# Performance work log

Hardware: AMD Instinct MI355X
Metric: run time of the kernel (lower is better)

The kernel has to match this reference:

```python
import jax, jax.numpy as jnp
import numpy as np

NUM_CODES = 8192
DIM = 512
COMMITMENT_COST = 0.25


def setup_inputs() -> dict:
    key = jax.random.key(0)
    kx, kc = jax.random.split(key)
    x = jax.random.normal(kx, (8, 4096, DIM), dtype=jnp.float32)
    # nn.init.uniform_(codebook.weight, -1/num_codes, 1/num_codes)
    bound = 1.0 / NUM_CODES
    codebook = jax.random.uniform(kc, (NUM_CODES, DIM), dtype=jnp.float32,
                                  minval=-bound, maxval=bound)
    return {"x": x, "codebook": codebook}


def reference(x, codebook):
    orig_shape = x.shape
    flat = x.reshape(-1, orig_shape[-1])              # [N, D]
    # Squared-distance expansion (argmin-equivalent to torch.cdist's L2):
    # ||f||^2 - 2 f.c + ||c||^2
    x_sq = jnp.sum(flat * flat, axis=-1, keepdims=True)          # [N, 1]
    c_sq = jnp.sum(codebook * codebook, axis=-1)                 # [K]
    dists = x_sq - 2.0 * jnp.einsum('nd,kd->nk', flat, codebook) + c_sq  # [N, K]
    indices_flat = jnp.argmin(dists, axis=-1)                    # [N] int
    quantized_flat = codebook[indices_flat]                      # [N, D]
    # codebook_loss = mse(quantized, sg(flat)); commitment = mse(flat, sg(quantized))
    codebook_loss = jnp.mean((quantized_flat - jax.lax.stop_gradient(flat)) ** 2)
    commitment_loss = jnp.mean((flat - jax.lax.stop_gradient(quantized_flat)) ** 2)
    vq_loss = codebook_loss + COMMITMENT_COST * commitment_loss
    # straight-through
    quantized_st = flat + jax.lax.stop_gradient(quantized_flat - flat)
    return (quantized_st.reshape(orig_shape), vq_loss,
            indices_flat.reshape(orig_shape[:-1]))
```

## Files before the change

kernel.cpp:

```cpp
#include <hip/hip_runtime.h>


#define NROWS 32768
#define KCODES 8192
#define DD 512
#define CAP 24
#define MARGIN 2.5e-4f

typedef __bf16 bf16_t;
typedef __bf16 bf16x8 __attribute__((ext_vector_type(8)));
typedef float f32x4 __attribute__((ext_vector_type(4)));

__device__ __forceinline__ int lofs(int row, int s) {
  return row * 32 + (((s ^ ((row >> 1) & 3))) << 3);
}

__device__ __forceinline__ void gld16(const bf16_t* g, bf16_t* l) {
  __builtin_amdgcn_global_load_lds(
      (const __attribute__((address_space(1))) void*)g,
      (__attribute__((address_space(3))) void*)l, 16, 0, 0);
}

__global__ __launch_bounds__(256) void prep_kernel(const float* __restrict__ in,
                                                   float* __restrict__ out_sq,
                                                   bf16_t* __restrict__ outb,
                                                   int nrows) {
  const int wave = threadIdx.x >> 6;
  const int lane = threadIdx.x & 63;
  const int row = blockIdx.x * 4 + wave;
  if (row >= nrows) return;
  const float* p = in + (size_t)row * DD;
  double s = 0.0;
#pragma unroll
  for (int j = 0; j < DD / 64; ++j) {
    float v = p[j * 64 + lane];
    float sq = v * v;
    s += (double)sq;
  }
  for (int off = 32; off > 0; off >>= 1) s += __shfl_down(s, off, 64);
  if (lane == 0) out_sq[row] = (float)s;
  const float4* p4 = (const float4*)p;
  float4 a = p4[lane * 2];
  float4 b = p4[lane * 2 + 1];
  bf16x8 o = {(bf16_t)a.x, (bf16_t)a.y, (bf16_t)a.z, (bf16_t)a.w,
              (bf16_t)b.x, (bf16_t)b.y, (bf16_t)b.z, (bf16_t)b.w};
  *(bf16x8*)(outb + (size_t)row * DD + lane * 8) = o;
}

__global__ __launch_bounds__(256, 3) void coarse_kernel(
    const bf16_t* __restrict__ xbf, const bf16_t* __restrict__ cbbf,
    const float* __restrict__ csq, unsigned char* __restrict__ cnt_g,
    unsigned short* __restrict__ list_g) {
  __shared__ bf16_t As[2][128 * 32];
  __shared__ bf16_t Bs[2][128 * 32];
  __shared__ unsigned best[128];
  __shared__ int cnt_l[128];
  __shared__ int list_l[128 * CAP];

  const int tid = threadIdx.x;
  const int w = tid >> 6;
  const int lane = tid & 63;
  const int q = lane >> 4;
  const int l15 = lane & 15;
  const int rOff = (w & 1) * 64;
  const int cOff = (w >> 1) * 64;

  const int bid = blockIdx.x;
  const int xcd = bid & 7;
  const int g = bid >> 3;
  const int qtr = xcd >> 1;
  const int rowblk = (xcd & 1) * 128 + g;
  const int row0 = rowblk * 128;
  const int cbase = qtr * (KCODES / 4);
  const int NCI = (KCODES / 4) / 128;
  const int NSTEP = NCI * (DD / 32);

  for (int i = tid; i < 128; i += 256) { best[i] = 0xFFFFFFFFu; cnt_l[i] = 0; }

  const int sub = lane >> 2;
  const int pos = lane & 3;
  const bf16_t *agp[2], *bgp[2];
  int aofs[2], bofs[2];
#pragma unroll
  for (int a = 0; a < 2; ++a) {
    const int row = w * 32 + a * 16 + sub;
    const int sg = pos ^ ((row >> 1) & 3);
    agp[a] = xbf + (size_t)(row0 + row) * DD + sg * 8;
    aofs[a] = row * 32 + pos * 8;
    bgp[a] = cbbf + (size_t)(cbase + row) * DD + sg * 8;
    bofs[a] = row * 32 + pos * 8;
  }

  int afofs[4], bfofs[4];
#pragma unroll
  for (int rt = 0; rt < 4; ++rt) afofs[rt] = lofs(rOff + rt * 16 + l15, q);
#pragma unroll
  for (int ct = 0; ct < 4; ++ct) bfofs[ct] = lofs(cOff + ct * 16 + l15, q);

  gld16(agp[0], &As[0][aofs[0]]);
  gld16(agp[1], &As[0][aofs[1]]);
  gld16(bgp[0], &Bs[0][bofs[0]]);
  gld16(bgp[1], &Bs[0][bofs[1]]);
  __syncthreads();

  f32x4 acc[4][4];

#define PIPE_STEP(S, CUR)                                                     \
  do {                                                                        \
    const int sN = (S) + 1;                                                   \
    if (sN < NSTEP) {                                                         \
      const int kbN = (sN & (DD / 32 - 1)) * 32;                              \
      const size_t coffN = (size_t)((sN >> 4) * 128) * DD;                    \
      gld16(agp[0] + kbN, &As[(CUR) ^ 1][aofs[0]]);                           \
      gld16(agp[1] + kbN, &As[(CUR) ^ 1][aofs[1]]);                           \
      gld16(bgp[0] + coffN + kbN, &Bs[(CUR) ^ 1][bofs[0]]);                   \
      gld16(bgp[1] + coffN + kbN, &Bs[(CUR) ^ 1][bofs[1]]);                   \
    }                                                                         \
    bf16x8 af[4], bfr[4];                                                     \
    _Pragma("unroll") for (int rt = 0; rt < 4; ++rt)                          \
        af[rt] = *(const bf16x8*)&As[(CUR)][afofs[rt]];                       \
    _Pragma("unroll") for (int ct = 0; ct < 4; ++ct)                          \
        bfr[ct] = *(const bf16x8*)&Bs[(CUR)][bfofs[ct]];                      \
    _Pragma("unroll") for (int rt = 0; rt < 4; ++rt)                          \
        _Pragma("unroll") for (int ct = 0; ct < 4; ++ct)                      \
            acc[rt][ct] = __builtin_amdgcn_mfma_f32_16x16x32_bf16(            \
                af[rt], bfr[ct], acc[rt][ct], 0, 0, 0);                       \
    asm volatile("s_waitcnt vmcnt(0)" ::: "memory");                          \
    __builtin_amdgcn_sched_barrier(0);                                        \
    __builtin_amdgcn_s_barrier();                                             \
    __builtin_amdgcn_sched_barrier(0);                                        \
  } while (0)

#pragma unroll 1
  for (int ci = 0; ci < NCI; ++ci) {
    const int c0 = cbase + ci * 128;
#pragma unroll
    for (int rt = 0; rt < 4; ++rt)
#pragma unroll
      for (int ct = 0; ct < 4; ++ct) {
        f32x4 z = {0.f, 0.f, 0.f, 0.f};
        acc[rt][ct] = z;
      }

#pragma unroll 1
    for (int kc2 = 0; kc2 < (DD / 32) / 2; ++kc2) {
      const int s = ci * (DD / 32) + kc2 * 2;
      PIPE_STEP(s, 0);
      PIPE_STEP(s + 1, 1);
    }

    float cs1[4];
#pragma unroll
    for (int ct = 0; ct < 4; ++ct)
      cs1[ct] = 1.0f + csq[c0 + cOff + ct * 16 + l15];

#pragma unroll
    for (int rt = 0; rt < 4; ++rt) {
#pragma unroll
      for (int reg = 0; reg < 4; ++reg) {
        float m = fmaf(-2.0f, acc[rt][0][reg], cs1[0]);
#pragma unroll
        for (int ct = 1; ct < 4; ++ct) {
          float d = fmaf(-2.0f, acc[rt][ct][reg], cs1[ct]);
          m = fminf(m, d);
        }
        unsigned mb = __float_as_uint(m);
#pragma unroll
        for (int msk = 1; msk <= 8; msk <<= 1) {
          unsigned o = __shfl_xor(mb, msk, 64);
          mb = mb < o ? mb : o;
        }
        if (l15 == 0) atomicMin(&best[rOff + rt * 16 + q * 4 + reg], mb);
      }
    }
    __syncthreads();

#pragma unroll
    for (int rt = 0; rt < 4; ++rt) {
#pragma unroll
      for (int reg = 0; reg < 4; ++reg) {
        const int rloc = rOff + rt * 16 + q * 4 + reg;
        const float thr = __uint_as_float(best[rloc]) + MARGIN;
#pragma unroll
        for (int ct = 0; ct < 4; ++ct) {
          float d = fmaf(-2.0f, acc[rt][ct][reg], cs1[ct]);
          if (d <= thr) {
            int pos2 = atomicAdd(&cnt_l[rloc], 1);
            if (pos2 < CAP)
              list_l[rloc * CAP + pos2] = c0 + cOff + ct * 16 + l15;
          }
        }
      }
    }
    __syncthreads();
  }
#undef PIPE_STEP

  for (int i = tid; i < 128; i += 256) {
    int c = cnt_l[i];
    cnt_g[(size_t)(row0 + i) * 4 + qtr] = (unsigned char)(c > CAP ? CAP + 1 : c);
  }
  for (int i = tid; i < 128 * CAP; i += 256) {
    const int r = i / CAP, p = i % CAP;
    list_g[((size_t)(row0 + r) * 4 + qtr) * CAP + p] =
        (unsigned short)list_l[i];
  }
}

__device__ __forceinline__ float exact_dist(const float4* __restrict__ xr4,
                                            const float* __restrict__ cb,
                                            const float* __restrict__ csq,
                                            float xs, int idx) {
  const float4* cr4 = (const float4*)(cb + (size_t)idx * DD);
  float acc = 0.0f;
  for (int k4 = 0; k4 < DD / 4; ++k4) {
    float4 xv = xr4[k4];
    float4 cv = cr4[k4];
    acc = fmaf(xv.x, cv.x, acc);
    acc = fmaf(xv.y, cv.y, acc);
    acc = fmaf(xv.z, cv.z, acc);
    acc = fmaf(xv.w, cv.w, acc);
  }
  float t = xs - 2.0f * acc;
  return t + csq[idx];
}

__global__ __launch_bounds__(256) void rescore_epilogue_kernel(
    const float* __restrict__ x, const float* __restrict__ cb,
    const float* __restrict__ xsq, const float* __restrict__ csq,
    const unsigned short* __restrict__ list,
    const unsigned char* __restrict__ cnt, float* __restrict__ out_q,
    float* __restrict__ out_idx_f, double* __restrict__ partials) {
  const int row = blockIdx.x * 4 + (threadIdx.x >> 6);
  const int lane = threadIdx.x & 63;
  const unsigned char* c4 = cnt + (size_t)row * 4;
  const float xs = xsq[row];
  const float4* xr4 = (const float4*)(x + (size_t)row * DD);

  int n[4];
  bool ok[4];
  int L = 0;
#pragma unroll
  for (int s = 0; s < 4; ++s) {
    n[s] = c4[s];
    ok[s] = (n[s] <= CAP);
    if (ok[s]) L += n[s];
  }
  if (L > 64 || L == 0) {
#pragma unroll
    for (int s = 0; s < 4; ++s) ok[s] = false;
    L = 0;
  }

  unsigned long long bestv = ~0ULL;

  int myidx = -1;
  int base = 0;
#pragma unroll
  for (int s = 0; s < 4; ++s) {
    if (ok[s]) {
      if (myidx < 0 && lane >= base && lane < base + n[s])
        myidx = (int)list[((size_t)row * 4 + s) * CAP + (lane - base)];
      base += n[s];
    }
  }
  if (myidx >= 0) {
    float d = exact_dist(xr4, cb, csq, xs, myidx);
    bestv = ((unsigned long long)__float_as_uint(d) << 32) | (unsigned)myidx;
  }

#pragma unroll
  for (int s = 0; s < 4; ++s) {
    if (!ok[s]) {
      const int q0 = s * (KCODES / 4);
      for (int idx = q0 + lane; idx < q0 + KCODES / 4; idx += 64) {
        float d = exact_dist(xr4, cb, csq, xs, idx);
        unsigned long long pk =
            ((unsigned long long)__float_as_uint(d) << 32) | (unsigned)idx;
        if (pk < bestv) bestv = pk;
      }
    }
  }

#pragma unroll
  for (int s = 1; s <= 32; s <<= 1) {
    unsigned long long o = __shfl_xor(bestv, s, 64);
    if (o < bestv) bestv = o;
  }
  const int k = (int)(bestv & 0xffffffffu);

  const float4* qr = (const float4*)(cb + (size_t)k * DD);
  float4* orow = (float4*)(out_q + (size_t)row * DD);

  float4 xa = xr4[lane], qa = qr[lane];
  float dax = qa.x - xa.x, day = qa.y - xa.y, daz = qa.z - xa.z, daw = qa.w - xa.w;
  float4 oa;
  oa.x = xa.x + dax; oa.y = xa.y + day; oa.z = xa.z + daz; oa.w = xa.w + daw;
  orow[lane] = oa;
  double pa = (double)(dax * dax) + (double)(day * day) +
              (double)(daz * daz) + (double)(daw * daw);

  float4 xb = xr4[lane + 64], qb = qr[lane + 64];
  float dbx = qb.x - xb.x, dby = qb.y - xb.y, dbz = qb.z - xb.z, dbw = qb.w - xb.w;
  float4 ob;
  ob.x = xb.x + dbx; ob.y = xb.y + dby; ob.z = xb.z + dbz; ob.w = xb.w + dbw;
  orow[lane + 64] = ob;
  double pb = (double)(dbx * dbx) + (double)(dby * dby) +
              (double)(dbz * dbz) + (double)(dbw * dbw);

  for (int off = 32; off > 0; off >>= 1) pa += __shfl_down(pa, off, 64);
  for (int off = 32; off > 0; off >>= 1) pb += __shfl_down(pb, off, 64);
  if (lane == 0) {
    partials[row] = pa + pb;
    out_idx_f[row] = (float)k;
  }
}

__global__ __launch_bounds__(256) void finalize_kernel(
    const double* __restrict__ partials, float* __restrict__ out_loss) {
  __shared__ double red[256];
  double s = 0.0;
  for (int i = threadIdx.x; i < NROWS; i += 256) s += partials[i];
  red[threadIdx.x] = s;
  __syncthreads();
  for (int st = 128; st > 0; st >>= 1) {
    if (threadIdx.x < st) red[threadIdx.x] += red[threadIdx.x + st];
    __syncthreads();
  }
  if (threadIdx.x == 0) {
    double mean = red[0] / ((double)NROWS * (double)DD);
    float cl = (float)mean;
    out_loss[0] = cl + 0.25f * cl;
  }
}

extern "C" void kernel_launch(void* const* d_in, const int* in_sizes, int n_in,
                              void* d_out, int out_size, void* d_ws,
                              size_t ws_size, hipStream_t stream) {
  const float* x = (const float*)d_in[0];
  const float* cb = (const float*)d_in[1];
  float* out = (float*)d_out;

  char* ws = (char*)d_ws;
  double* partials = (double*)ws;
  float* csq = (float*)(ws + 262144);
  float* xsq = (float*)(ws + 262144 + 32768);
  unsigned char* cnt = (unsigned char*)(ws + 262144 + 32768 + 131072);
  unsigned short* list =
      (unsigned short*)(ws + 262144 + 32768 + 131072 + 131072);

  bf16_t* cbbf = (bf16_t*)d_out;
  bf16_t* xbf = cbbf + (size_t)KCODES * DD;

  prep_kernel<<<KCODES / 4, 256, 0, stream>>>(cb, csq, cbbf, KCODES);
  prep_kernel<<<NROWS / 4, 256, 0, stream>>>(x, xsq, xbf, NROWS);
  coarse_kernel<<<1024, 256, 0, stream>>>(xbf, cbbf, csq, cnt, list);
  rescore_epilogue_kernel<<<NROWS / 4, 256, 0, stream>>>(
      x, cb, xsq, csq, list, cnt, out, out + 16777216 + 1, partials);
  finalize_kernel<<<1, 256, 0, stream>>>(partials, out + 16777216);
}
```

Before: 1.010 ms.

## Deepen coarse GEMM pipeline to four stages and prune rescore quarters by global minimum

The coarse bf16 GEMM kernel moves from a two-buffer to a four-buffer LDS ring with three loads in flight, and waits on a partial vmcnt instead of draining all loads each step. It also drops one block barrier per code tile and stores the candidate list as shorts. Each quarter's coarse minimum is now written out, so the rescore kernel can skip quarters whose minimum exceeds the global minimum plus margin, avoiding full scans of irrelevant quarters. The cost is more LDS per block and lower occupancy (launch bound 3 to 2). Removing the per-tile barrier could race on best/cnt_l between iterations.

```diff
diff --git a/kernel.cpp b/kernel.cpp
--- a/kernel.cpp
+++ b/kernel.cpp
@@ -47,15 +47,15 @@
   *(bf16x8*)(outb + (size_t)row * DD + lane * 8) = o;
 }
 
-__global__ __launch_bounds__(256, 3) void coarse_kernel(
+__global__ __launch_bounds__(256, 2) void coarse_kernel(
     const bf16_t* __restrict__ xbf, const bf16_t* __restrict__ cbbf,
     const float* __restrict__ csq, unsigned char* __restrict__ cnt_g,
-    unsigned short* __restrict__ list_g) {
-  __shared__ bf16_t As[2][128 * 32];
-  __shared__ bf16_t Bs[2][128 * 32];
+    unsigned short* __restrict__ list_g, unsigned* __restrict__ bmin_g) {
+  __shared__ bf16_t As[4][128 * 32];
+  __shared__ bf16_t Bs[4][128 * 32];
   __shared__ unsigned best[128];
   __shared__ int cnt_l[128];
-  __shared__ int list_l[128 * CAP];
+  __shared__ unsigned short list_l[128 * CAP];
 
   const int tid = threadIdx.x;
   const int w = tid >> 6;
@@ -73,7 +73,6 @@
   const int row0 = rowblk * 128;
   const int cbase = qtr * (KCODES / 4);
   const int NCI = (KCODES / 4) / 128;
-  const int NSTEP = NCI * (DD / 32);
 
   for (int i = tid; i < 128; i += 256) { best[i] = 0xFFFFFFFFu; cnt_l[i] = 0; }
 
@@ -97,35 +96,38 @@
 #pragma unroll
   for (int ct = 0; ct < 4; ++ct) bfofs[ct] = lofs(cOff + ct * 16 + l15, q);
 
-  gld16(agp[0], &As[0][aofs[0]]);
-  gld16(agp[1], &As[0][aofs[1]]);
-  gld16(bgp[0], &Bs[0][bofs[0]]);
-  gld16(bgp[1], &Bs[0][bofs[1]]);
-  __syncthreads();
+  auto issue_step = [&](int sN, int buf) {
+    const int kbN = (sN & (DD / 32 - 1)) * 32;
+    const size_t coffN = (size_t)((sN >> 4) & (NCI - 1)) * (128 * DD);
+    gld16(agp[0] + kbN, &As[buf][aofs[0]]);
+    gld16(agp[1] + kbN, &As[buf][aofs[1]]);
+    gld16(bgp[0] + coffN + kbN, &Bs[buf][bofs[0]]);
+    gld16(bgp[1] + coffN + kbN, &Bs[buf][bofs[1]]);
+  };
+
+  issue_step(0, 0);
+  issue_step(1, 1);
+  issue_step(2, 2);
+  asm volatile("s_waitcnt vmcnt(8) lgkmcnt(0)" ::: "memory");
+  __builtin_amdgcn_sched_barrier(0);
+  __builtin_amdgcn_s_barrier();
+  __builtin_amdgcn_sched_barrier(0);
 
   f32x4 acc[4][4];
 
-#define PIPE_STEP(S, CUR)                                                     \
+#define PIPE_STEP(S, J)                                                       \
   do {                                                                        \
-    const int sN = (S) + 1;                                                   \
-    if (sN < NSTEP) {                                                         \
-      const int kbN = (sN & (DD / 32 - 1)) * 32;                              \
-      const size_t coffN = (size_t)((sN >> 4) * 128) * DD;                    \
-      gld16(agp[0] + kbN, &As[(CUR) ^ 1][aofs[0]]);                           \
-      gld16(agp[1] + kbN, &As[(CUR) ^ 1][aofs[1]]);                           \
-      gld16(bgp[0] + coffN + kbN, &Bs[(CUR) ^ 1][bofs[0]]);                   \
-      gld16(bgp[1] + coffN + kbN, &Bs[(CUR) ^ 1][bofs[1]]);                   \
-    }                                                                         \
+    issue_step((S) + 3, ((J) + 3) & 3);                                       \
     bf16x8 af[4], bfr[4];                                                     \
     _Pragma("unroll") for (int rt = 0; rt < 4; ++rt)                          \
-        af[rt] = *(const bf16x8*)&As[(CUR)][afofs[rt]];                       \
+        af[rt] = *(const bf16x8*)&As[(J)][afofs[rt]];                         \
     _Pragma("unroll") for (int ct = 0; ct < 4; ++ct)                          \
-        bfr[ct] = *(const bf16x8*)&Bs[(CUR)][bfofs[ct]];                      \
+        bfr[ct] = *(const bf16x8*)&Bs[(J)][bfofs[ct]];                        \
     _Pragma("unroll") for (int rt = 0; rt < 4; ++rt)                          \
         _Pragma("unroll") for (int ct = 0; ct < 4; ++ct)                      \
             acc[rt][ct] = __builtin_amdgcn_mfma_f32_16x16x32_bf16(            \
                 af[rt], bfr[ct], acc[rt][ct], 0, 0, 0);                       \
-    asm volatile("s_waitcnt vmcnt(0)" ::: "memory");                          \
+    asm volatile("s_waitcnt vmcnt(8)" ::: "memory");                          \
     __builtin_amdgcn_sched_barrier(0);                                        \
     __builtin_amdgcn_s_barrier();                                             \
     __builtin_amdgcn_sched_barrier(0);                                        \
@@ -143,10 +145,12 @@
       }
 
 #pragma unroll 1
-    for (int kc2 = 0; kc2 < (DD / 32) / 2; ++kc2) {
-      const int s = ci * (DD / 32) + kc2 * 2;
-      PIPE_STEP(s, 0);
+    for (int kc4 = 0; kc4 < 4; ++kc4) {
+      const int s = ci * 16 + kc4 * 4;
+      PIPE_STEP(s + 0, 0);
       PIPE_STEP(s + 1, 1);
+      PIPE_STEP(s + 2, 2);
+      PIPE_STEP(s + 3, 3);
     }
 
     float cs1[4];
@@ -173,7 +177,10 @@
         if (l15 == 0) atomicMin(&best[rOff + rt * 16 + q * 4 + reg], mb);
       }
     }
-    __syncthreads();
+    asm volatile("s_waitcnt lgkmcnt(0)" ::: "memory");
+    __builtin_amdgcn_sched_barrier(0);
+    __builtin_amdgcn_s_barrier();
+    __builtin_amdgcn_sched_barrier(0);
 
 #pragma unroll
     for (int rt = 0; rt < 4; ++rt) {
@@ -187,23 +194,25 @@
           if (d <= thr) {
             int pos2 = atomicAdd(&cnt_l[rloc], 1);
             if (pos2 < CAP)
-              list_l[rloc * CAP + pos2] = c0 + cOff + ct * 16 + l15;
+              list_l[rloc * CAP + pos2] =
+                  (unsigned short)(c0 + cOff + ct * 16 + l15);
           }
         }
       }
     }
-    __syncthreads();
   }
 #undef PIPE_STEP
+
+  __syncthreads();
 
   for (int i = tid; i < 128; i += 256) {
     int c = cnt_l[i];
     cnt_g[(size_t)(row0 + i) * 4 + qtr] = (unsigned char)(c > CAP ? CAP + 1 : c);
+    bmin_g[(size_t)(row0 + i) * 4 + qtr] = best[i];
   }
   for (int i = tid; i < 128 * CAP; i += 256) {
     const int r = i / CAP, p = i % CAP;
-    list_g[((size_t)(row0 + r) * 4 + qtr) * CAP + p] =
-        (unsigned short)list_l[i];
+    list_g[((size_t)(row0 + r) * 4 + qtr) * CAP + p] = list_l[i];
   }
 }
 
@@ -229,26 +238,38 @@
     const float* __restrict__ x, const float* __restrict__ cb,
     const float* __restrict__ xsq, const float* __restrict__ csq,
     const unsigned short* __restrict__ list,
-    const unsigned char* __restrict__ cnt, float* __restrict__ out_q,
-    float* __restrict__ out_idx_f, double* __restrict__ partials) {
+    const unsigned char* __restrict__ cnt, const unsigned* __restrict__ bmin,
+    float* __restrict__ out_q, float* __restrict__ out_idx_f,
+    double* __restrict__ partials) {
   const int row = blockIdx.x * 4 + (threadIdx.x >> 6);
   const int lane = threadIdx.x & 63;
   const unsigned char* c4 = cnt + (size_t)row * 4;
+  const unsigned* bm4 = bmin + (size_t)row * 4;
   const float xs = xsq[row];
   const float4* xr4 = (const float4*)(x + (size_t)row * DD);
 
+  float qm[4];
   int n[4];
-  bool ok[4];
+#pragma unroll
+  for (int s = 0; s < 4; ++s) {
+    qm[s] = __uint_as_float(bm4[s]);
+    n[s] = c4[s];
+  }
+  const float gmin = fminf(fminf(qm[0], qm[1]), fminf(qm[2], qm[3]));
+  const float cut = gmin + MARGIN;
+  bool listed[4], scanq[4];
   int L = 0;
 #pragma unroll
   for (int s = 0; s < 4; ++s) {
-    n[s] = c4[s];
-    ok[s] = (n[s] <= CAP);
-    if (ok[s]) L += n[s];
-  }
-  if (L > 64 || L == 0) {
-#pragma unroll
-    for (int s = 0; s < 4; ++s) ok[s] = false;
+    const bool rel = (qm[s] <= cut);
+    listed[s] = rel && (n[s] <= CAP);
+    scanq[s] = rel && (n[s] > CAP);
+    if (listed[s]) L += n[s];
+  }
+  if (L > 64) {
+#pragma unroll
+    for (int s = 0; s < 4; ++s)
+      if (listed[s]) { listed[s] = false; scanq[s] = true; }
     L = 0;
   }
 
@@ -258,7 +279,7 @@
   int base = 0;
 #pragma unroll
   for (int s = 0; s < 4; ++s) {
-    if (ok[s]) {
+    if (listed[s]) {
       if (myidx < 0 && lane >= base && lane < base + n[s])
         myidx = (int)list[((size_t)row * 4 + s) * CAP + (lane - base)];
       base += n[s];
@@ -271,7 +292,7 @@
 
 #pragma unroll
   for (int s = 0; s < 4; ++s) {
-    if (!ok[s]) {
+    if (scanq[s]) {
       const int q0 = s * (KCODES / 4);
       for (int idx = q0 + lane; idx < q0 + KCODES / 4; idx += 64) {
         float d = exact_dist(xr4, cb, csq, xs, idx);
@@ -346,16 +367,17 @@
   float* csq = (float*)(ws + 262144);
   float* xsq = (float*)(ws + 262144 + 32768);
   unsigned char* cnt = (unsigned char*)(ws + 262144 + 32768 + 131072);
+  unsigned* bmin = (unsigned*)(ws + 262144 + 32768 + 131072 + 131072);
   unsigned short* list =
-      (unsigned short*)(ws + 262144 + 32768 + 131072 + 131072);
+      (unsigned short*)(ws + 262144 + 32768 + 131072 + 131072 + 524288);
 
   bf16_t* cbbf = (bf16_t*)d_out;
   bf16_t* xbf = cbbf + (size_t)KCODES * DD;
 
   prep_kernel<<<KCODES / 4, 256, 0, stream>>>(cb, csq, cbbf, KCODES);
   prep_kernel<<<NROWS / 4, 256, 0, stream>>>(x, xsq, xbf, NROWS);
-  coarse_kernel<<<1024, 256, 0, stream>>>(xbf, cbbf, csq, cnt, list);
+  coarse_kernel<<<1024, 256, 0, stream>>>(xbf, cbbf, csq, cnt, list, bmin);
   rescore_epilogue_kernel<<<NROWS / 4, 256, 0, stream>>>(
-      x, cb, xsq, csq, list, cnt, out, out + 16777216 + 1, partials);
+      x, cb, xsq, csq, list, cnt, bmin, out, out + 16777216 + 1, partials);
   finalize_kernel<<<1, 256, 0, stream>>>(partials, out + 16777216);
 }
```

New measurement: 1.007 ms. About the same (-0.3%).
